# Performance work log

Hardware: AMD Instinct MI355X
Metric: run time of the kernel (lower is better)

The kernel has to match this reference:

```python
import jax, jax.numpy as jnp
import numpy as np

INPUT_SIZE = 256
IN_CH = 1536
OUT_CH = 1536
B = 8


def patchify(f):
    # F.unfold(k=3, p=1, s=1) -> [B, L, C, 3, 3] with L = H*W (PyTorch channel order c,ki,kj)
    Bn, C, H, W = f.shape
    p = jnp.pad(f, ((0, 0), (0, 0), (1, 1), (1, 1)))
    shifts = [p[:, :, i:i + H, j:j + W] for i in range(3) for j in range(3)]
    patches = jnp.stack(shifts, axis=2)                 # [B, C, 9, H, W]
    patches = patches.reshape(Bn, C, 3, 3, H, W)
    patches = patches.transpose(0, 4, 5, 1, 2, 3)       # [B, H, W, C, 3, 3]
    return patches.reshape(Bn, H * W, C, 3, 3)


def adaptive_pool(y, out):
    # equals F.adaptive_avg_pool1d when L % out == 0 (guaranteed by our dims)
    N, L = y.shape
    return y.reshape(N, out, L // out).mean(-1)


def setup_inputs():
    key = jax.random.key(0)
    k1, k2, k3, k4 = jax.random.split(key, 4)
    s0, s1 = INPUT_SIZE // 8, INPUT_SIZE // 16
    x0 = jax.random.normal(k1, (B, 512, s0, s0), dtype=jnp.float32)
    x1 = jax.random.normal(k2, (B, 1024, s1, s1), dtype=jnp.float32)
    # xavier_normal: std = sqrt(2/(fan_in+fan_out))
    W = jax.random.normal(k3, (OUT_CH, IN_CH), dtype=jnp.float32) * (2.0 / (IN_CH + OUT_CH)) ** 0.5
    b = jax.random.normal(k4, (OUT_CH,), dtype=jnp.float32) * 0.01
    return {"x0": x0, "x1": x1, "W": W, "b": b}


def reference(x0, x1, W, b):
    Bn = x0.shape[0]
    s0 = x0.shape[-1]              # input_size // 8
    s1 = x1.shape[-1]              # input_size // 16
    C1 = x1.shape[1]

    p0 = patchify(x0)              # [B, s0*s0, 512, 3, 3]
    p1 = patchify(x1)              # [B, s1*s1, 1024, 3, 3]

    # upsample the level-1 patch grid (s1,s1) -> (s0,s0), bilinear align_corners=False
    y = p1.reshape(Bn, s1, s1, C1, 3, 3).transpose(0, 3, 4, 5, 1, 2)   # [B, C1, 3, 3, s1, s1]
    y = y.reshape(Bn * C1 * 9, s1, s1)
    y = jax.image.resize(y, (Bn * C1 * 9, s0, s0), method='bilinear')
    y = y.reshape(Bn, C1, 3, 3, s0, s0).transpose(0, 4, 5, 1, 2, 3)    # [B, s0, s0, C1, 3, 3]
    p1 = y.reshape(Bn, s0 * s0, C1, 3, 3)

    feats = []
    for p in (p0, p1):
        f = p.reshape(-1, p.shape[-3] * 9)        # [B*s0*s0, C*9]
        feats.append(adaptive_pool(f, IN_CH))     # [B*s0*s0, IN_CH]
    x = jnp.stack(feats, axis=1).reshape(-1, 2 * IN_CH)
    x = adaptive_pool(x, IN_CH)                   # [B*s0*s0, IN_CH]
    return x @ W.T + b                            # [B*s0*s0, OUT_CH]
```

## Files before the change

### kernel.cpp

```cpp
#include <hip/hip_runtime.h>
#include <hip/hip_bf16.h>


typedef __bf16 bf16x8 __attribute__((ext_vector_type(8)));
typedef float  f32x4  __attribute__((ext_vector_type(4)));
typedef const void __attribute__((address_space(1)))* gptr_t;
typedef void __attribute__((address_space(3)))* sptr_t;

#define M_TOT 8192
#define N_TOT 1536
#define K_TOT 1536

__global__ __launch_bounds__(256) void prep_kernel(const float* __restrict__ x1,
                                                   const float* __restrict__ W,
                                                   float* __restrict__ q1,
                                                   __hip_bfloat16* __restrict__ Wb) {
  __shared__ float T[128 * 3 * 16];
  __shared__ __align__(16) float outT[16 * 100];
  const int bid = blockIdx.x;
  const int tid = threadIdx.x;

  if (bid >= 1024) {
    int i = ((bid - 1024) * 256 + tid) * 4;
    float4 v = *(const float4*)(W + i);
    Wb[i + 0] = __float2bfloat16(v.x);
    Wb[i + 1] = __float2bfloat16(v.y);
    Wb[i + 2] = __float2bfloat16(v.z);
    Wb[i + 3] = __float2bfloat16(v.w);
    return;
  }
  const int cb = bid & 7, sh = (bid >> 3) & 15, b = bid >> 7;
  const float* xb = x1 + (size_t)(b * 1024 + cb * 128) * 256;

#pragma unroll
  for (int i = 0; i < 24; ++i) {
    int v = tid + i * 256;
    int c = v / 48, rem = v - c * 48;
    int y = rem >> 4, w = rem & 15;
    int gy = sh + y - 1;
    float s = 0.f;
    if (gy >= 0 && gy < 16) {
      const float* row = xb + (c * 16 + gy) * 16;
      s = row[w];
      if (w > 0)  s += row[w - 1];
      if (w < 15) s += row[w + 1];
    }
    T[v] = s;
  }
  __syncthreads();

  const int w = tid & 15, mg = tid >> 4;
#pragma unroll
  for (int k = 0; k < 6; ++k) {
    int ml = mg * 6 + k;
    int tl = ml / 3, p = ml - 3 * tl;
    const float* Tb = T + (4 * tl) * 48;
    float s;
    if (p == 0)      s = Tb[w]       + Tb[16 + w]  + Tb[32 + w]  + Tb[48 + w];
    else if (p == 1) s = Tb[64 + w]  + Tb[80 + w]  + Tb[96 + w]  + Tb[112 + w];
    else             s = Tb[128 + w] + Tb[144 + w] + Tb[160 + w] + Tb[176 + w];
    outT[w * 100 + ml] = s * (1.f / 12.f);
  }
  __syncthreads();

#pragma unroll
  for (int i = 0; i < 2; ++i) {
    int q = tid + i * 256;
    if (q < 384) {
      int nl = q / 24, qc = q - nl * 24;
      float4 v4 = *(const float4*)&outT[nl * 100 + qc * 4];
      *(float4*)&q1[(size_t)(b * 256 + sh * 16 + nl) * 768 + cb * 96 + qc * 4] = v4;
    }
  }
}

__global__ __launch_bounds__(256) void featx_kernel(const float* __restrict__ x0,
                                                    const float* __restrict__ q1,
                                                    __hip_bfloat16* __restrict__ X) {
  __shared__ float T[64 * 3 * 32];
  __shared__ __align__(16) unsigned short outT[32 * 100];
  const int bid = blockIdx.x;
  const int tid = threadIdx.x;

  if (bid >= 2048) {
    int idx = (bid - 2048) * 256 + tid;
    int mg = idx % 192;
    int n = idx / 192;
    int w = n & 31, h = (n >> 5) & 31, b = n >> 10;

    int th = h >> 1, tw = w >> 1;
    int i0, i1, j0, j1;
    float wh0, wh1, wv0, wv1;
    if ((h & 1) == 0) { i0 = th - 1; i1 = th;     wh0 = 0.25f; wh1 = 0.75f; }
    else              { i0 = th;     i1 = th + 1; wh0 = 0.75f; wh1 = 0.25f; }
    if ((w & 1) == 0) { j0 = tw - 1; j1 = tw;     wv0 = 0.25f; wv1 = 0.75f; }
    else              { j0 = tw;     j1 = tw + 1; wv0 = 0.75f; wv1 = 0.25f; }
    if (i0 < 0) i0 = 0; if (i1 > 15) i1 = 15;
    if (j0 < 0) j0 = 0; if (j1 > 15) j1 = 15;

    const float* q = q1 + (size_t)b * 196608 + mg * 4;
    float4 s00 = *(const float4*)&q[(i0 * 16 + j0) * 768];
    float4 s01 = *(const float4*)&q[(i0 * 16 + j1) * 768];
    float4 s10 = *(const float4*)&q[(i1 * 16 + j0) * 768];
    float4 s11 = *(const float4*)&q[(i1 * 16 + j1) * 768];

    float4 v;
    v.x = wh0 * (wv0 * s00.x + wv1 * s01.x) + wh1 * (wv0 * s10.x + wv1 * s11.x);
    v.y = wh0 * (wv0 * s00.y + wv1 * s01.y) + wh1 * (wv0 * s10.y + wv1 * s11.y);
    v.z = wh0 * (wv0 * s00.z + wv1 * s01.z) + wh1 * (wv0 * s10.z + wv1 * s11.z);
    v.w = wh0 * (wv0 * s00.w + wv1 * s01.w) + wh1 * (wv0 * s10.w + wv1 * s11.w);

    ushort4 o;
    __hip_bfloat16 t0 = __float2bfloat16(v.x); o.x = *(unsigned short*)&t0;
    __hip_bfloat16 t1 = __float2bfloat16(v.y); o.y = *(unsigned short*)&t1;
    __hip_bfloat16 t2 = __float2bfloat16(v.z); o.z = *(unsigned short*)&t2;
    __hip_bfloat16 t3 = __float2bfloat16(v.w); o.w = *(unsigned short*)&t3;
    *(ushort4*)&X[(size_t)n * 1536 + 768 + mg * 4] = o;
    return;
  }

  const int cb = bid & 7, h = (bid >> 3) & 31, b = bid >> 8;
  const float* xb = x0 + (size_t)(b * 512 + cb * 64) * 1024;

#pragma unroll
  for (int i = 0; i < 24; ++i) {
    int v = tid + i * 256;
    int c = v / 96, rem = v - c * 96;
    int y = rem >> 5, w = rem & 31;
    int gy = h + y - 1;
    float s = 0.f;
    if (gy >= 0 && gy < 32) {
      const float* row = xb + (c * 32 + gy) * 32;
      s = row[w];
      if (w > 0)  s += row[w - 1];
      if (w < 31) s += row[w + 1];
    }
    T[v] = s;
  }
  __syncthreads();

  const int w = tid & 31, og = tid >> 5;
#pragma unroll
  for (int k = 0; k < 12; ++k) {
    int ol = og * 12 + k;
    int tl = ol / 3, p = ol - 3 * tl;
    const float* Tb = T + (2 * tl) * 96;
    float s;
    if (p == 0)      s = Tb[w]       + Tb[32 + w];
    else if (p == 1) s = Tb[64 + w]  + Tb[96 + w];
    else             s = Tb[128 + w] + Tb[160 + w];
    __hip_bfloat16 hv = __float2bfloat16(s * (1.f / 6.f));
    outT[w * 100 + ol] = *(unsigned short*)&hv;
  }
  __syncthreads();

#pragma unroll
  for (int i = 0; i < 3; ++i) {
    int q = tid + i * 256;
    int nl = q / 24, qc = q - nl * 24;
    ushort4 v4 = *(const ushort4*)&outT[nl * 100 + qc * 4];
    *(ushort4*)&X[(size_t)(b * 1024 + h * 32 + nl) * 1536 + cb * 96 + qc * 4] = v4;
  }
}

#define SLICES 48

__global__ __launch_bounds__(512, 2) void gemm_kernel(
    const __hip_bfloat16* __restrict__ Xg,
    const __hip_bfloat16* __restrict__ Wg,
    const float* __restrict__ bias,
    float* __restrict__ out) {
  __shared__ __align__(16) __hip_bfloat16 ringA[4][256 * 32];
  __shared__ __align__(16) __hip_bfloat16 ringB[4][256 * 32];

  const int tid = threadIdx.x;
  const int lane = tid & 63;
  const int wave = tid >> 6;
  const int wm = wave >> 2;
  const int wn = wave & 3;

  const int bid = blockIdx.x;
  const int swz = (bid & 7) * 24 + (bid >> 3);
  const int tileN = (swz % 6) * 256;
  const int tileM = (swz / 6) * 256;

  const int r0 = tid >> 2;
  const int sc = (tid & 3) ^ ((r0 >> 1) & 3);
  const __hip_bfloat16* srcA0 = Xg + (size_t)(tileM + r0) * K_TOT + sc * 8;
  const __hip_bfloat16* srcA1 = srcA0 + (size_t)128 * K_TOT;
  const __hip_bfloat16* srcB0 = Wg + (size_t)(tileN + r0) * K_TOT + sc * 8;
  const __hip_bfloat16* srcB1 = srcB0 + (size_t)128 * K_TOT;

  int aoff[8], boff[4];
#pragma unroll
  for (int mf = 0; mf < 8; ++mf) {
    int row = wm * 128 + mf * 16 + (lane & 15);
    int pg = (lane >> 4) ^ ((row >> 1) & 3);
    aoff[mf] = (row * 4 + pg) * 8;
  }
#pragma unroll
  for (int nf = 0; nf < 4; ++nf) {
    int row = wn * 64 + nf * 16 + (lane & 15);
    int pg = (lane >> 4) ^ ((row >> 1) & 3);
    boff[nf] = (row * 4 + pg) * 8;
  }

  f32x4 acc[8][4] = {};

#define STAGE(slot, s)                                                          \
  {                                                                             \
    __builtin_amdgcn_global_load_lds((gptr_t)(srcA0 + (s) * 32),                \
        (sptr_t)(&ringA[slot][tid * 8]), 16, 0, 0);                             \
    __builtin_amdgcn_global_load_lds((gptr_t)(srcA1 + (s) * 32),                \
        (sptr_t)(&ringA[slot][(tid + 512) * 8]), 16, 0, 0);                     \
    __builtin_amdgcn_global_load_lds((gptr_t)(srcB0 + (s) * 32),                \
        (sptr_t)(&ringB[slot][tid * 8]), 16, 0, 0);                             \
    __builtin_amdgcn_global_load_lds((gptr_t)(srcB1 + (s) * 32),                \
        (sptr_t)(&ringB[slot][(tid + 512) * 8]), 16, 0, 0);                     \
  }

#define BODY(slot)                                                              \
  {                                                                             \
    bf16x8 af[8], bf[4];                                                        \
    _Pragma("unroll")                                                           \
    for (int mf = 0; mf < 8; ++mf)                                              \
      af[mf] = *(const bf16x8*)(&ringA[slot][aoff[mf]]);                        \
    _Pragma("unroll")                                                           \
    for (int nf = 0; nf < 4; ++nf)                                              \
      bf[nf] = *(const bf16x8*)(&ringB[slot][boff[nf]]);                        \
    __builtin_amdgcn_s_setprio(1);                                              \
    _Pragma("unroll")                                                           \
    for (int mf = 0; mf < 8; ++mf)                                              \
      _Pragma("unroll")                                                         \
      for (int nf = 0; nf < 4; ++nf)                                            \
        acc[mf][nf] = __builtin_amdgcn_mfma_f32_16x16x32_bf16(                  \
            af[mf], bf[nf], acc[mf][nf], 0, 0, 0);                              \
    __builtin_amdgcn_s_setprio(0);                                              \
  }

#define OPEN(vm)                                                                \
  asm volatile("s_waitcnt vmcnt(" #vm ")" ::: "memory");                        \
  __builtin_amdgcn_s_barrier();                                                 \
  __builtin_amdgcn_sched_barrier(0);

#define CLOSE                                                                   \
  __builtin_amdgcn_sched_barrier(0);                                            \
  __builtin_amdgcn_s_barrier();                                                 \
  __builtin_amdgcn_sched_barrier(0);

  STAGE(0, 0) STAGE(1, 1) STAGE(2, 2)

#pragma unroll 4
  for (int s = 0; s < SLICES - 4; ++s) {
    STAGE((s + 3) & 3, s + 3)
    OPEN(12)
    BODY(s & 3)
    CLOSE
  }
  STAGE(3, 47)
  OPEN(12) BODY(0) CLOSE
  OPEN(8)  BODY(1) CLOSE
  OPEN(4)  BODY(2) CLOSE
  OPEN(0)  BODY(3)

  const int colbase = tileN + wn * 64 + (lane & 15);
  const int rowbase = tileM + wm * 128 + ((lane >> 4) << 2);
#pragma unroll
  for (int mf = 0; mf < 8; ++mf) {
#pragma unroll
    for (int nf = 0; nf < 4; ++nf) {
      int col = colbase + nf * 16;
      float bv = bias[col];
#pragma unroll
      for (int r = 0; r < 4; ++r) {
        int row = rowbase + mf * 16 + r;
        out[(size_t)row * N_TOT + col] = acc[mf][nf][r] + bv;
      }
    }
  }
#undef STAGE
#undef BODY
#undef OPEN
#undef CLOSE
}

extern "C" void kernel_launch(void* const* d_in, const int* in_sizes, int n_in,
                              void* d_out, int out_size, void* d_ws, size_t ws_size,
                              hipStream_t stream) {
  const float* x0 = (const float*)d_in[0];
  const float* x1 = (const float*)d_in[1];
  const float* W = (const float*)d_in[2];
  const float* bias = (const float*)d_in[3];
  float* out = (float*)d_out;

  char* ws = (char*)d_ws;
  __hip_bfloat16* X = (__hip_bfloat16*)ws;
  __hip_bfloat16* Wb = (__hip_bfloat16*)(ws + 25165824);
  float* q1 = (float*)(ws + 25165824 + 4718592);

  prep_kernel<<<3328, 256, 0, stream>>>(x1, W, q1, Wb);
  featx_kernel<<<8192, 256, 0, stream>>>(x0, q1, X);
  gemm_kernel<<<192, 512, 0, stream>>>(X, Wb, bias, out);
}
```

Before: 179.4 us.

## Apply level-1 GEMM before bilinear upsampling and fuse upsample into epilogue

Bilinear upsampling is linear, so the level-1 features are multiplied by their half of W at low resolution (2048 rows instead of 8192). The result is then upsampled inside the main GEMM epilogue, which now only runs over K=768. This removes a quarter of the GEMM FLOPs and the full-resolution upsampled feature write. The two feature-prep kernels are also merged into one launch. The cost is an extra small GEMM launch and four gathered fp32 reads per output element in the epilogue.

```diff
diff --git a/kernel.cpp b/kernel.cpp
--- a/kernel.cpp
+++ b/kernel.cpp
@@ -7,21 +7,22 @@
 typedef const void __attribute__((address_space(1)))* gptr_t;
 typedef void __attribute__((address_space(3)))* sptr_t;
 
-#define M_TOT 8192
 #define N_TOT 1536
-#define K_TOT 1536
-
-__global__ __launch_bounds__(256) void prep_kernel(const float* __restrict__ x1,
+#define KP 768
+
+__global__ __launch_bounds__(256) void prep_kernel(const float* __restrict__ x0,
+                                                   const float* __restrict__ x1,
                                                    const float* __restrict__ W,
-                                                   float* __restrict__ q1,
+                                                   __hip_bfloat16* __restrict__ X0,
+                                                   __hip_bfloat16* __restrict__ q1b,
                                                    __hip_bfloat16* __restrict__ Wb) {
-  __shared__ float T[128 * 3 * 16];
-  __shared__ __align__(16) float outT[16 * 100];
+  __shared__ float T[6144];
+  __shared__ __align__(16) unsigned short outT[3200];
   const int bid = blockIdx.x;
   const int tid = threadIdx.x;
 
-  if (bid >= 1024) {
-    int i = ((bid - 1024) * 256 + tid) * 4;
+  if (bid >= 3072) {
+    int i = ((bid - 3072) * 256 + tid) * 4;
     float4 v = *(const float4*)(W + i);
     Wb[i + 0] = __float2bfloat16(v.x);
     Wb[i + 1] = __float2bfloat16(v.y);
@@ -29,97 +30,57 @@
     Wb[i + 3] = __float2bfloat16(v.w);
     return;
   }
-  const int cb = bid & 7, sh = (bid >> 3) & 15, b = bid >> 7;
-  const float* xb = x1 + (size_t)(b * 1024 + cb * 128) * 256;
-
-#pragma unroll
-  for (int i = 0; i < 24; ++i) {
-    int v = tid + i * 256;
-    int c = v / 48, rem = v - c * 48;
-    int y = rem >> 4, w = rem & 15;
-    int gy = sh + y - 1;
-    float s = 0.f;
-    if (gy >= 0 && gy < 16) {
-      const float* row = xb + (c * 16 + gy) * 16;
-      s = row[w];
-      if (w > 0)  s += row[w - 1];
-      if (w < 15) s += row[w + 1];
-    }
-    T[v] = s;
-  }
-  __syncthreads();
-
-  const int w = tid & 15, mg = tid >> 4;
-#pragma unroll
-  for (int k = 0; k < 6; ++k) {
-    int ml = mg * 6 + k;
-    int tl = ml / 3, p = ml - 3 * tl;
-    const float* Tb = T + (4 * tl) * 48;
-    float s;
-    if (p == 0)      s = Tb[w]       + Tb[16 + w]  + Tb[32 + w]  + Tb[48 + w];
-    else if (p == 1) s = Tb[64 + w]  + Tb[80 + w]  + Tb[96 + w]  + Tb[112 + w];
-    else             s = Tb[128 + w] + Tb[144 + w] + Tb[160 + w] + Tb[176 + w];
-    outT[w * 100 + ml] = s * (1.f / 12.f);
-  }
-  __syncthreads();
-
-#pragma unroll
-  for (int i = 0; i < 2; ++i) {
-    int q = tid + i * 256;
-    if (q < 384) {
-      int nl = q / 24, qc = q - nl * 24;
-      float4 v4 = *(const float4*)&outT[nl * 100 + qc * 4];
-      *(float4*)&q1[(size_t)(b * 256 + sh * 16 + nl) * 768 + cb * 96 + qc * 4] = v4;
-    }
-  }
-}
-
-__global__ __launch_bounds__(256) void featx_kernel(const float* __restrict__ x0,
-                                                    const float* __restrict__ q1,
-                                                    __hip_bfloat16* __restrict__ X) {
-  __shared__ float T[64 * 3 * 32];
-  __shared__ __align__(16) unsigned short outT[32 * 100];
-  const int bid = blockIdx.x;
-  const int tid = threadIdx.x;
-
-  if (bid >= 2048) {
-    int idx = (bid - 2048) * 256 + tid;
-    int mg = idx % 192;
-    int n = idx / 192;
-    int w = n & 31, h = (n >> 5) & 31, b = n >> 10;
-
-    int th = h >> 1, tw = w >> 1;
-    int i0, i1, j0, j1;
-    float wh0, wh1, wv0, wv1;
-    if ((h & 1) == 0) { i0 = th - 1; i1 = th;     wh0 = 0.25f; wh1 = 0.75f; }
-    else              { i0 = th;     i1 = th + 1; wh0 = 0.75f; wh1 = 0.25f; }
-    if ((w & 1) == 0) { j0 = tw - 1; j1 = tw;     wv0 = 0.25f; wv1 = 0.75f; }
-    else              { j0 = tw;     j1 = tw + 1; wv0 = 0.75f; wv1 = 0.25f; }
-    if (i0 < 0) i0 = 0; if (i1 > 15) i1 = 15;
-    if (j0 < 0) j0 = 0; if (j1 > 15) j1 = 15;
-
-    const float* q = q1 + (size_t)b * 196608 + mg * 4;
-    float4 s00 = *(const float4*)&q[(i0 * 16 + j0) * 768];
-    float4 s01 = *(const float4*)&q[(i0 * 16 + j1) * 768];
-    float4 s10 = *(const float4*)&q[(i1 * 16 + j0) * 768];
-    float4 s11 = *(const float4*)&q[(i1 * 16 + j1) * 768];
-
-    float4 v;
-    v.x = wh0 * (wv0 * s00.x + wv1 * s01.x) + wh1 * (wv0 * s10.x + wv1 * s11.x);
-    v.y = wh0 * (wv0 * s00.y + wv1 * s01.y) + wh1 * (wv0 * s10.y + wv1 * s11.y);
-    v.z = wh0 * (wv0 * s00.z + wv1 * s01.z) + wh1 * (wv0 * s10.z + wv1 * s11.z);
-    v.w = wh0 * (wv0 * s00.w + wv1 * s01.w) + wh1 * (wv0 * s10.w + wv1 * s11.w);
-
-    ushort4 o;
-    __hip_bfloat16 t0 = __float2bfloat16(v.x); o.x = *(unsigned short*)&t0;
-    __hip_bfloat16 t1 = __float2bfloat16(v.y); o.y = *(unsigned short*)&t1;
-    __hip_bfloat16 t2 = __float2bfloat16(v.z); o.z = *(unsigned short*)&t2;
-    __hip_bfloat16 t3 = __float2bfloat16(v.w); o.w = *(unsigned short*)&t3;
-    *(ushort4*)&X[(size_t)n * 1536 + 768 + mg * 4] = o;
+
+  if (bid < 1024) {
+    const int cb = bid & 7, sh = (bid >> 3) & 15, b = bid >> 7;
+    const float* xb = x1 + (size_t)(b * 1024 + cb * 128) * 256;
+
+#pragma unroll
+    for (int i = 0; i < 24; ++i) {
+      int v = tid + i * 256;
+      int c = v / 48, rem = v - c * 48;
+      int y = rem >> 4, w = rem & 15;
+      int gy = sh + y - 1;
+      float s = 0.f;
+      if (gy >= 0 && gy < 16) {
+        const float* row = xb + (c * 16 + gy) * 16;
+        s = row[w];
+        if (w > 0)  s += row[w - 1];
+        if (w < 15) s += row[w + 1];
+      }
+      T[v] = s;
+    }
+    __syncthreads();
+
+    const int w = tid & 15, mg = tid >> 4;
+#pragma unroll
+    for (int k = 0; k < 6; ++k) {
+      int ml = mg * 6 + k;
+      int tl = ml / 3, p = ml - 3 * tl;
+      const float* Tb = T + (4 * tl) * 48;
+      float s;
+      if (p == 0)      s = Tb[w]       + Tb[16 + w]  + Tb[32 + w]  + Tb[48 + w];
+      else if (p == 1) s = Tb[64 + w]  + Tb[80 + w]  + Tb[96 + w]  + Tb[112 + w];
+      else             s = Tb[128 + w] + Tb[144 + w] + Tb[160 + w] + Tb[176 + w];
+      __hip_bfloat16 hv = __float2bfloat16(s * (1.f / 12.f));
+      outT[w * 100 + ml] = *(unsigned short*)&hv;
+    }
+    __syncthreads();
+
+#pragma unroll
+    for (int i = 0; i < 2; ++i) {
+      int q = tid + i * 256;
+      if (q < 384) {
+        int nl = q / 24, qc = q - nl * 24;
+        ushort4 v4 = *(const ushort4*)&outT[nl * 100 + qc * 4];
+        *(ushort4*)&q1b[(size_t)(b * 256 + sh * 16 + nl) * KP + cb * 96 + qc * 4] = v4;
+      }
+    }
     return;
   }
 
-  const int cb = bid & 7, h = (bid >> 3) & 31, b = bid >> 8;
+  const int fb = bid - 1024;
+  const int cb = fb & 7, h = (fb >> 3) & 31, b = fb >> 8;
   const float* xb = x0 + (size_t)(b * 512 + cb * 64) * 1024;
 
 #pragma unroll
@@ -159,16 +120,114 @@
     int q = tid + i * 256;
     int nl = q / 24, qc = q - nl * 24;
     ushort4 v4 = *(const ushort4*)&outT[nl * 100 + qc * 4];
-    *(ushort4*)&X[(size_t)(b * 1024 + h * 32 + nl) * 1536 + cb * 96 + qc * 4] = v4;
+    *(ushort4*)&X0[(size_t)(b * 1024 + h * 32 + nl) * KP + cb * 96 + qc * 4] = v4;
   }
 }
 
-#define SLICES 48
-
-__global__ __launch_bounds__(512, 2) void gemm_kernel(
+#define G1_NT 12
+
+__global__ __launch_bounds__(256) void gemm1_kernel(
+    const __hip_bfloat16* __restrict__ Ag,
+    const __hip_bfloat16* __restrict__ Bg,
+    float* __restrict__ Yg) {
+  __shared__ __align__(16) __hip_bfloat16 As[2][128 * 64];
+  __shared__ __align__(16) __hip_bfloat16 Bs[2][128 * 64];
+
+  const int tid = threadIdx.x;
+  const int lane = tid & 63;
+  const int wave = tid >> 6;
+  const int wr = wave >> 1, wc = wave & 1;
+
+  int id = blockIdx.y * gridDim.x + blockIdx.x;
+  int swz = (id & 7) * 24 + (id >> 3);
+  const int tileN = (swz % 12) * 128;
+  const int tileM = (swz / 12) * 128;
+
+  const int srow = tid >> 3;
+  const int scol = (((tid & 7) ^ ((tid >> 3) & 7)) << 3);
+
+  f32x4 acc[4][4] = {};
+
+#define STAGE1(buf, k0)                                                         \
+  { _Pragma("unroll")                                                           \
+    for (int i = 0; i < 4; ++i) {                                               \
+      int row = i * 32 + srow;                                                  \
+      __builtin_amdgcn_global_load_lds(                                         \
+          (gptr_t)(Ag + (size_t)(tileM + row) * KP + (k0) + scol),              \
+          (sptr_t)(&As[buf][i * 2048 + tid * 8]), 16, 0, 0);                    \
+    }                                                                           \
+    _Pragma("unroll")                                                           \
+    for (int i = 0; i < 4; ++i) {                                               \
+      int row = i * 32 + srow;                                                  \
+      __builtin_amdgcn_global_load_lds(                                         \
+          (gptr_t)(Bg + (size_t)(tileN + row) * N_TOT + (k0) + scol),           \
+          (sptr_t)(&Bs[buf][i * 2048 + tid * 8]), 16, 0, 0);                    \
+    } }
+
+#define COMPUTE1(buf)                                                           \
+  { const __hip_bfloat16* as = &As[buf][0];                                     \
+    const __hip_bfloat16* bs = &Bs[buf][0];                                     \
+    _Pragma("unroll")                                                           \
+    for (int kk = 0; kk < 64; kk += 32) {                                       \
+      bf16x8 afr[4], bfr[4];                                                    \
+      int kq = (kk >> 3) + (lane >> 4);                                         \
+      int pg = kq ^ (lane & 7);                                                 \
+      _Pragma("unroll")                                                         \
+      for (int mf = 0; mf < 4; ++mf) {                                          \
+        int row = wr * 64 + mf * 16 + (lane & 15);                              \
+        afr[mf] = *(const bf16x8*)(as + row * 64 + pg * 8);                     \
+      }                                                                         \
+      _Pragma("unroll")                                                         \
+      for (int nf = 0; nf < 4; ++nf) {                                          \
+        int col = wc * 64 + nf * 16 + (lane & 15);                              \
+        bfr[nf] = *(const bf16x8*)(bs + col * 64 + pg * 8);                     \
+      }                                                                         \
+      _Pragma("unroll")                                                         \
+      for (int mf = 0; mf < 4; ++mf)                                            \
+        _Pragma("unroll")                                                       \
+        for (int nf = 0; nf < 4; ++nf)                                          \
+          acc[mf][nf] = __builtin_amdgcn_mfma_f32_16x16x32_bf16(                \
+              afr[mf], bfr[nf], acc[mf][nf], 0, 0, 0);                          \
+    } }
+
+  STAGE1(0, 0)
+  for (int t = 0; t < G1_NT - 1; ++t) {
+    STAGE1((t + 1) & 1, (t + 1) * 64)
+    asm volatile("s_waitcnt vmcnt(8)" ::: "memory");
+    __builtin_amdgcn_s_barrier();
+    __builtin_amdgcn_sched_barrier(0);
+    COMPUTE1(t & 1)
+    __builtin_amdgcn_sched_barrier(0);
+    asm volatile("" ::: "memory");
+    __builtin_amdgcn_s_barrier();
+  }
+  asm volatile("s_waitcnt vmcnt(0)" ::: "memory");
+  __builtin_amdgcn_s_barrier();
+  __builtin_amdgcn_sched_barrier(0);
+  COMPUTE1((G1_NT - 1) & 1)
+
+  const int colbase = tileN + wc * 64 + (lane & 15);
+  const int rowbase = tileM + wr * 64 + ((lane >> 4) << 2);
+#pragma unroll
+  for (int mf = 0; mf < 4; ++mf)
+#pragma unroll
+    for (int nf = 0; nf < 4; ++nf) {
+      int col = colbase + nf * 16;
+#pragma unroll
+      for (int r = 0; r < 4; ++r)
+        Yg[(size_t)(rowbase + mf * 16 + r) * N_TOT + col] = acc[mf][nf][r];
+    }
+#undef STAGE1
+#undef COMPUTE1
+}
+
+#define SLICES 24
+
+__global__ __launch_bounds__(512, 2) void gemm0_kernel(
     const __hip_bfloat16* __restrict__ Xg,
     const __hip_bfloat16* __restrict__ Wg,
     const float* __restrict__ bias,
+    const float* __restrict__ y1,
     float* __restrict__ out) {
   __shared__ __align__(16) __hip_bfloat16 ringA[4][256 * 32];
   __shared__ __align__(16) __hip_bfloat16 ringB[4][256 * 32];
@@ -186,10 +245,10 @@
 
   const int r0 = tid >> 2;
   const int sc = (tid & 3) ^ ((r0 >> 1) & 3);
-  const __hip_bfloat16* srcA0 = Xg + (size_t)(tileM + r0) * K_TOT + sc * 8;
-  const __hip_bfloat16* srcA1 = srcA0 + (size_t)128 * K_TOT;
-  const __hip_bfloat16* srcB0 = Wg + (size_t)(tileN + r0) * K_TOT + sc * 8;
-  const __hip_bfloat16* srcB1 = srcB0 + (size_t)128 * K_TOT;
+  const __hip_bfloat16* srcA0 = Xg + (size_t)(tileM + r0) * KP + sc * 8;
+  const __hip_bfloat16* srcA1 = srcA0 + (size_t)128 * KP;
+  const __hip_bfloat16* srcB0 = Wg + (size_t)(tileN + r0) * N_TOT + sc * 8;
+  const __hip_bfloat16* srcB1 = srcB0 + (size_t)128 * N_TOT;
 
   int aoff[8], boff[4];
 #pragma unroll
@@ -208,20 +267,17 @@
   f32x4 acc[8][4] = {};
 
 #define STAGE(slot, s)                                                          \
-  {                                                                             \
-    __builtin_amdgcn_global_load_lds((gptr_t)(srcA0 + (s) * 32),                \
+  { __builtin_amdgcn_global_load_lds((gptr_t)(srcA0 + (s) * 32),                \
         (sptr_t)(&ringA[slot][tid * 8]), 16, 0, 0);                             \
     __builtin_amdgcn_global_load_lds((gptr_t)(srcA1 + (s) * 32),                \
         (sptr_t)(&ringA[slot][(tid + 512) * 8]), 16, 0, 0);                     \
     __builtin_amdgcn_global_load_lds((gptr_t)(srcB0 + (s) * 32),                \
         (sptr_t)(&ringB[slot][tid * 8]), 16, 0, 0);                             \
     __builtin_amdgcn_global_load_lds((gptr_t)(srcB1 + (s) * 32),                \
-        (sptr_t)(&ringB[slot][(tid + 512) * 8]), 16, 0, 0);                     \
-  }
+        (sptr_t)(&ringB[slot][(tid + 512) * 8]), 16, 0, 0); }
 
 #define BODY(slot)                                                              \
-  {                                                                             \
-    bf16x8 af[8], bf[4];                                                        \
+  { bf16x8 af[8], bf[4];                                                        \
     _Pragma("unroll")                                                           \
     for (int mf = 0; mf < 8; ++mf)                                              \
       af[mf] = *(const bf16x8*)(&ringA[slot][aoff[mf]]);                        \
@@ -235,8 +291,7 @@
       for (int nf = 0; nf < 4; ++nf)                                            \
         acc[mf][nf] = __builtin_amdgcn_mfma_f32_16x16x32_bf16(                  \
             af[mf], bf[nf], acc[mf][nf], 0, 0, 0);                              \
-    __builtin_amdgcn_s_setprio(0);                                              \
-  }
+    __builtin_amdgcn_s_setprio(0); }
 
 #define OPEN(vm)                                                                \
   asm volatile("s_waitcnt vmcnt(" #vm ")" ::: "memory");                        \
@@ -257,7 +312,7 @@
     BODY(s & 3)
     CLOSE
   }
-  STAGE(3, 47)
+  STAGE(3, SLICES - 1)
   OPEN(12) BODY(0) CLOSE
   OPEN(8)  BODY(1) CLOSE
   OPEN(4)  BODY(2) CLOSE
@@ -265,16 +320,34 @@
 
   const int colbase = tileN + wn * 64 + (lane & 15);
   const int rowbase = tileM + wm * 128 + ((lane >> 4) << 2);
+  float bv[4];
+#pragma unroll
+  for (int nf = 0; nf < 4; ++nf) bv[nf] = bias[colbase + nf * 16];
+
 #pragma unroll
   for (int mf = 0; mf < 8; ++mf) {
 #pragma unroll
-    for (int nf = 0; nf < 4; ++nf) {
-      int col = colbase + nf * 16;
-      float bv = bias[col];
-#pragma unroll
-      for (int r = 0; r < 4; ++r) {
-        int row = rowbase + mf * 16 + r;
-        out[(size_t)row * N_TOT + col] = acc[mf][nf][r] + bv;
+    for (int r = 0; r < 4; ++r) {
+      int row = rowbase + mf * 16 + r;
+      int w = row & 31, h = (row >> 5) & 31, b = row >> 10;
+      int th = h >> 1, tw = w >> 1;
+      int i0, i1, j0, j1;
+      float wh0, wh1, wv0, wv1;
+      if ((h & 1) == 0) { i0 = th - 1; i1 = th;     wh0 = 0.25f; wh1 = 0.75f; }
+      else              { i0 = th;     i1 = th + 1; wh0 = 0.75f; wh1 = 0.25f; }
+      if ((w & 1) == 0) { j0 = tw - 1; j1 = tw;     wv0 = 0.25f; wv1 = 0.75f; }
+      else              { j0 = tw;     j1 = tw + 1; wv0 = 0.75f; wv1 = 0.25f; }
+      if (i0 < 0) i0 = 0; if (i1 > 15) i1 = 15;
+      if (j0 < 0) j0 = 0; if (j1 > 15) j1 = 15;
+      const float* yr0 = y1 + (size_t)(b * 256 + i0 * 16) * N_TOT;
+      const float* yr1 = y1 + (size_t)(b * 256 + i1 * 16) * N_TOT;
+      float w00 = wh0 * wv0, w01 = wh0 * wv1, w10 = wh1 * wv0, w11 = wh1 * wv1;
+#pragma unroll
+      for (int nf = 0; nf < 4; ++nf) {
+        int col = colbase + nf * 16;
+        float up = w00 * yr0[j0 * N_TOT + col] + w01 * yr0[j1 * N_TOT + col] +
+                   w10 * yr1[j0 * N_TOT + col] + w11 * yr1[j1 * N_TOT + col];
+        out[(size_t)row * N_TOT + col] = acc[mf][nf][r] + up + bv[nf];
       }
     }
   }
@@ -294,11 +367,12 @@
   float* out = (float*)d_out;
 
   char* ws = (char*)d_ws;
-  __hip_bfloat16* X = (__hip_bfloat16*)ws;
-  __hip_bfloat16* Wb = (__hip_bfloat16*)(ws + 25165824);
-  float* q1 = (float*)(ws + 25165824 + 4718592);
-
-  prep_kernel<<<3328, 256, 0, stream>>>(x1, W, q1, Wb);
-  featx_kernel<<<8192, 256, 0, stream>>>(x0, q1, X);
-  gemm_kernel<<<192, 512, 0, stream>>>(X, Wb, bias, out);
+  __hip_bfloat16* X0 = (__hip_bfloat16*)ws;
+  __hip_bfloat16* Wb = (__hip_bfloat16*)(ws + 12582912);
+  __hip_bfloat16* q1b = (__hip_bfloat16*)(ws + 17301504);
+  float* y1 = (float*)(ws + 20447232);
+
+  prep_kernel<<<5376, 256, 0, stream>>>(x0, x1, W, X0, q1b, Wb);
+  gemm1_kernel<<<dim3(12, 16), 256, 0, stream>>>(q1b, Wb + 768, y1);
+  gemm0_kernel<<<192, 512, 0, stream>>>(X0, Wb, bias, y1, out);
 }
```

New measurement: 177.0 us. About the same (-1.4%).
